# Performance work log

Measured on AMD Instinct MI355X. Metric: run time of the kernel, lower is better.

The kernel has to match this reference:

```python
import jax, jax.numpy as jnp
import numpy as np

B, TQ, TK, D = 16, 1024, 4096, 512


def setup_inputs() -> dict:
    key = jax.random.key(0)
    k1, k2, k3 = jax.random.split(key, 3)
    decoder_output = jax.random.normal(k1, (B, TQ, D), dtype=jnp.float32)
    encoder_output = jax.random.normal(k2, (B, TK, D), dtype=jnp.float32)
    # Keras Dense(lstm_size): kernel [D, D] (glorot-ish scale), bias [D] (zeros init)
    W_a = jax.random.normal(k3, (D, D), dtype=jnp.float32) * (1.0 / np.sqrt(D))
    b_a = jnp.zeros((D,), dtype=jnp.float32)
    return {"decoder_output": decoder_output, "encoder_output": encoder_output,
            "W_a": W_a, "b_a": b_a}


def reference(decoder_output, encoder_output, W_a, b_a):
    # Luong 'general' attention:
    # proj = Dense(encoder_output)            [B, Tk, D]
    proj = jnp.einsum('bkd,de->bke', encoder_output, W_a) + b_a
    # score = dec @ proj^T                    [B, Tq, Tk]
    score = jnp.einsum('bqd,bkd->bqk', decoder_output, proj)
    # softmax over encoder time axis (tf axis=2 == last axis here)
    alignment_vector = jax.nn.softmax(score, axis=-1)
    # context = align @ encoder_output        [B, Tq, D]
    context_vector = jnp.einsum('bqk,bkd->bqd', alignment_vector, encoder_output)
    return (context_vector, alignment_vector)
```

## Files before the change

### kernel.cpp

```cpp
#include <hip/hip_runtime.h>
#include <hip/hip_bf16.h>

#define B_  16
#define TQ_ 1024
#define TK_ 4096
#define D_  512

typedef unsigned short u16;
typedef __attribute__((ext_vector_type(8))) short short8;
typedef __attribute__((ext_vector_type(8))) _Float16 f16x8;
typedef __attribute__((ext_vector_type(4))) float f32x4;

__device__ __forceinline__ u16 bf16_rne(float x) {
  unsigned u = __float_as_uint(x);
  u += 0x7FFFu + ((u >> 16) & 1u);
  return (u16)(u >> 16);
}
__device__ __forceinline__ float bf16_as_f32(u16 h) {
  return __uint_as_float(((unsigned)h) << 16);
}
__device__ __forceinline__ void split_bf16(float x, u16& h, u16& l) {
  u16 hh = bf16_rne(x);
  h = hh;
  l = bf16_rne(x - bf16_as_f32(hh));
}

__device__ __forceinline__ void glld16(const void* g, void* lds) {
  __builtin_amdgcn_global_load_lds(
      (const __attribute__((address_space(1))) unsigned int*)g,
      (__attribute__((address_space(3))) unsigned int*)lds, 16, 0, 0);
}

__device__ __forceinline__ int seg_src4(int l) {
  return (l & 3) ^ ((l >> 2) & 3) ^ ((l >> 4) & 3);
}

__global__ __launch_bounds__(256) void split_planes_kernel(
    const float* __restrict__ X, u16* __restrict__ H, u16* __restrict__ L,
    int n8)
{
  int i = blockIdx.x * 256 + threadIdx.x;
  if (i >= n8) return;
  const float4* src = (const float4*)X + (size_t)i * 2;
  float4 a = src[0], b = src[1];
  __align__(16) u16 h[8], l[8];
  split_bf16(a.x, h[0], l[0]);
  split_bf16(a.y, h[1], l[1]);
  split_bf16(a.z, h[2], l[2]);
  split_bf16(a.w, h[3], l[3]);
  split_bf16(b.x, h[4], l[4]);
  split_bf16(b.y, h[5], l[5]);
  split_bf16(b.z, h[6], l[6]);
  split_bf16(b.w, h[7], l[7]);
  *(uint4*)&H[(size_t)i * 8] = *(const uint4*)h;
  *(uint4*)&L[(size_t)i * 8] = *(const uint4*)l;
}

__global__ __launch_bounds__(256) void transpose_conv_kernel(
    const float* __restrict__ E, _Float16* __restrict__ ET,
    _Float16* __restrict__ EF)
{
  __shared__ float tile[64][65];
  const int b  = blockIdx.z;
  const int k0 = blockIdx.x * 64;
  const int d0 = blockIdx.y * 64;
  const float* Eb = E + (long long)b * TK_ * D_;
  _Float16* ETb = ET + (long long)b * D_ * TK_;

  const int t  = threadIdx.x;
  const int r  = t >> 2;
  const int c4 = (t & 3) * 16;

  __align__(16) _Float16 g[16];
  #pragma unroll
  for (int i = 0; i < 16; i += 4) {
    float4 v = *(const float4*)&Eb[(long long)(k0 + r) * D_ + d0 + c4 + i];
    tile[r][c4 + i + 0] = v.x;
    tile[r][c4 + i + 1] = v.y;
    tile[r][c4 + i + 2] = v.z;
    tile[r][c4 + i + 3] = v.w;
    g[i + 0] = (_Float16)v.x;
    g[i + 1] = (_Float16)v.y;
    g[i + 2] = (_Float16)v.z;
    g[i + 3] = (_Float16)v.w;
  }
  if (EF) {
    _Float16* EFb = EF + (long long)b * TK_ * D_;
    uint4* dstF = (uint4*)&EFb[(long long)(k0 + r) * D_ + d0 + c4];
    dstF[0] = ((const uint4*)g)[0];
    dstF[1] = ((const uint4*)g)[1];
  }
  __syncthreads();

  __align__(16) _Float16 h[16];
  #pragma unroll
  for (int i = 0; i < 16; ++i) h[i] = (_Float16)tile[c4 + i][r];
  uint4* dst = (uint4*)&ETb[(long long)(d0 + r) * TK_ + k0 + c4];
  dst[0] = ((const uint4*)h)[0];
  dst[1] = ((const uint4*)h)[1];
}

#define D2BM 64
#define D2BN 128
#define D2BK 32

__global__ __launch_bounds__(256) void gemm_dec2p_kernel(
    const u16* __restrict__ Ahp, const u16* __restrict__ Alp,
    const u16* __restrict__ Bhp, const u16* __restrict__ Blp,
    _Float16* __restrict__ Ch, _Float16* __restrict__ Cl)
{
  __shared__ u16 sAh[D2BM * D2BK];
  __shared__ u16 sAl[D2BM * D2BK];
  __shared__ u16 sBh[D2BN * D2BK];
  __shared__ u16 sBl[D2BN * D2BK];

  const int m0 = blockIdx.y * D2BM;
  const int n0 = blockIdx.x * D2BN;

  const int t    = threadIdx.x;
  const int lane = t & 63;
  const int wave = t >> 6;
  const int wrm  = (wave >> 1) * 32;
  const int wcn  = (wave & 1) * 64;
  const int ln   = lane & 15;
  const int qd   = lane >> 4;
  const int sw   = qd ^ (ln & 3) ^ (ln >> 2);

  f32x4 acc[2][4];
  #pragma unroll
  for (int i = 0; i < 2; ++i)
    #pragma unroll
    for (int j = 0; j < 4; ++j) { f32x4 z = {0.f,0.f,0.f,0.f}; acc[i][j] = z; }

  const int ab = seg_src4(lane) * 16;
  const char* gAh = (const char*)Ahp + (long long)(m0 + wave * 16 + (lane >> 2)) * D_ * 2 + ab;
  const char* gAl = (const char*)Alp + (long long)(m0 + wave * 16 + (lane >> 2)) * D_ * 2 + ab;
  const int adst = wave * 1024 + lane * 16;
  const char* gBh = (const char*)Bhp + (long long)(n0 + wave * 32 + (lane >> 2)) * D_ * 2 + ab;
  const char* gBl = (const char*)Blp + (long long)(n0 + wave * 32 + (lane >> 2)) * D_ * 2 + ab;
  const long long rstep = (long long)16 * D_ * 2;
  const int bdst = wave * 2048 + lane * 16;

  for (int k0 = 0; k0 < D_; k0 += D2BK) {
    const long long ko = (long long)k0 * 2;
    glld16(gAh + ko, (char*)sAh + adst);
    glld16(gAl + ko, (char*)sAl + adst);
    glld16(gBh + ko, (char*)sBh + bdst);
    glld16(gBh + ko + rstep, (char*)sBh + bdst + 1024);
    glld16(gBl + ko, (char*)sBl + bdst);
    glld16(gBl + ko + rstep, (char*)sBl + bdst + 1024);
    __syncthreads();

    short8 fah[2], fal[2], fbh[4], fbl[4];
    #pragma unroll
    for (int i = 0; i < 2; ++i) {
      const int ra = (wrm + i * 16 + ln) * D2BK + sw * 8;
      fah[i] = *(const short8*)&sAh[ra];
      fal[i] = *(const short8*)&sAl[ra];
    }
    #pragma unroll
    for (int j = 0; j < 4; ++j) {
      const int rb = (wcn + j * 16 + ln) * D2BK + sw * 8;
      fbh[j] = *(const short8*)&sBh[rb];
      fbl[j] = *(const short8*)&sBl[rb];
    }
    #pragma unroll
    for (int i = 0; i < 2; ++i)
      #pragma unroll
      for (int j = 0; j < 4; ++j) {
        acc[i][j] = __builtin_amdgcn_mfma_f32_16x16x32_bf16(fah[i], fbh[j], acc[i][j], 0, 0, 0);
        acc[i][j] = __builtin_amdgcn_mfma_f32_16x16x32_bf16(fah[i], fbl[j], acc[i][j], 0, 0, 0);
        acc[i][j] = __builtin_amdgcn_mfma_f32_16x16x32_bf16(fal[i], fbh[j], acc[i][j], 0, 0, 0);
      }
    __syncthreads();
  }

  #pragma unroll
  for (int i = 0; i < 2; ++i)
    #pragma unroll
    for (int j = 0; j < 4; ++j)
      #pragma unroll
      for (int rg = 0; rg < 4; ++rg) {
        int row = m0 + wrm + i * 16 + qd * 4 + rg;
        int col = n0 + wcn + j * 16 + ln;
        float x = acc[i][j][rg];
        _Float16 h = (_Float16)x;
        _Float16 l = (_Float16)(x - (float)h);
        long long idx = (long long)row * D_ + col;
        Ch[idx] = h;
        Cl[idx] = l;
      }
}

#define DBM 128
#define DBN 128
#define DBK 32
#define DPAD 40

__global__ __launch_bounds__(256) void gemm_dec2_kernel(
    const float* __restrict__ A, const float* __restrict__ Bm,
    _Float16* __restrict__ Ch, _Float16* __restrict__ Cl)
{
  __shared__ u16 Ah[DBM * DPAD];
  __shared__ u16 Al[DBM * DPAD];
  __shared__ u16 Bh[DBN * DPAD];
  __shared__ u16 Bl[DBN * DPAD];

  const float* Ab = A  + (long long)(blockIdx.y * DBM) * D_;
  const float* Bb = Bm + (long long)(blockIdx.x * DBN) * D_;

  const int t    = threadIdx.x;
  const int r    = t >> 1;
  const int hf   = t & 1;
  const int lane = t & 63;
  const int wave = t >> 6;
  const int wr   = (wave >> 1) * 64;
  const int wc   = (wave & 1) * 64;
  const int ln   = lane & 15;
  const int qd   = lane >> 4;

  f32x4 acc[4][4];
  #pragma unroll
  for (int i = 0; i < 4; ++i)
    #pragma unroll
    for (int j = 0; j < 4; ++j) { f32x4 z = {0.f,0.f,0.f,0.f}; acc[i][j] = z; }

  const float* srcA = Ab + (long long)r * D_ + hf * 16;
  const float* srcB = Bb + (long long)r * D_ + hf * 16;
  u16* dAh = &Ah[r * DPAD + hf * 16];
  u16* dAl = &Al[r * DPAD + hf * 16];
  u16* dBh = &Bh[r * DPAD + hf * 16];
  u16* dBl = &Bl[r * DPAD + hf * 16];

  for (int k0 = 0; k0 < D_; k0 += DBK) {
    {
      __align__(16) u16 h[16], l[16];
      #pragma unroll
      for (int i = 0; i < 16; i += 4) {
        float4 v = *(const float4*)(srcA + k0 + i);
        split_bf16(v.x, h[i+0], l[i+0]);
        split_bf16(v.y, h[i+1], l[i+1]);
        split_bf16(v.z, h[i+2], l[i+2]);
        split_bf16(v.w, h[i+3], l[i+3]);
      }
      ((uint4*)dAh)[0] = ((const uint4*)h)[0];
      ((uint4*)dAh)[1] = ((const uint4*)h)[1];
      ((uint4*)dAl)[0] = ((const uint4*)l)[0];
      ((uint4*)dAl)[1] = ((const uint4*)l)[1];
      #pragma unroll
      for (int i = 0; i < 16; i += 4) {
        float4 v = *(const float4*)(srcB + k0 + i);
        split_bf16(v.x, h[i+0], l[i+0]);
        split_bf16(v.y, h[i+1], l[i+1]);
        split_bf16(v.z, h[i+2], l[i+2]);
        split_bf16(v.w, h[i+3], l[i+3]);
      }
      ((uint4*)dBh)[0] = ((const uint4*)h)[0];
      ((uint4*)dBh)[1] = ((const uint4*)h)[1];
      ((uint4*)dBl)[0] = ((const uint4*)l)[0];
      ((uint4*)dBl)[1] = ((const uint4*)l)[1];
    }
    __syncthreads();

    short8 fah[4], fal[4], fbh[4], fbl[4];
    #pragma unroll
    for (int i = 0; i < 4; ++i) {
      int ra = (wr + i * 16 + ln) * DPAD + qd * 8;
      int rb = (wc + i * 16 + ln) * DPAD + qd * 8;
      fah[i] = *(const short8*)&Ah[ra];
      fal[i] = *(const short8*)&Al[ra];
      fbh[i] = *(const short8*)&Bh[rb];
      fbl[i] = *(const short8*)&Bl[rb];
    }
    #pragma unroll
    for (int i = 0; i < 4; ++i)
      #pragma unroll
      for (int j = 0; j < 4; ++j) {
        acc[i][j] = __builtin_amdgcn_mfma_f32_16x16x32_bf16(fah[i], fbh[j], acc[i][j], 0, 0, 0);
        acc[i][j] = __builtin_amdgcn_mfma_f32_16x16x32_bf16(fah[i], fbl[j], acc[i][j], 0, 0, 0);
        acc[i][j] = __builtin_amdgcn_mfma_f32_16x16x32_bf16(fal[i], fbh[j], acc[i][j], 0, 0, 0);
      }
    __syncthreads();
  }

  const int m0 = blockIdx.y * DBM;
  const int n0 = blockIdx.x * DBN;
  #pragma unroll
  for (int i = 0; i < 4; ++i)
    #pragma unroll
    for (int j = 0; j < 4; ++j)
      #pragma unroll
      for (int rg = 0; rg < 4; ++rg) {
        int row = m0 + wr + i * 16 + qd * 4 + rg;
        int col = n0 + wc + j * 16 + ln;
        float x = acc[i][j][rg];
        _Float16 h = (_Float16)x;
        _Float16 l = (_Float16)(x - (float)h);
        long long idx = (long long)row * D_ + col;
        Ch[idx] = h;
        Cl[idx] = l;
      }
}

#define SBM 128
#define SBN 128
#define SBK 32

template<bool F16B>
__global__ __launch_bounds__(256) void gemm_score_kernel(
    const _Float16* __restrict__ A_h, const _Float16* __restrict__ A_l,
    const float* __restrict__ Bf, const _Float16* __restrict__ B16,
    float* __restrict__ C)
{
  __shared__ _Float16 sAh[SBM * SBK];
  __shared__ _Float16 sAl[SBM * SBK];
  __shared__ _Float16 sB [SBN * SBK];

  const int bz = blockIdx.z;
  const int m0 = blockIdx.y * SBM;
  const int n0 = blockIdx.x * SBN;
  const _Float16* Ahb = A_h + (long long)bz * TQ_ * D_ + (long long)m0 * D_;
  const _Float16* Alb = A_l + (long long)bz * TQ_ * D_ + (long long)m0 * D_;

  const int t    = threadIdx.x;
  const int lane = t & 63;
  const int wave = t >> 6;
  const int wr   = (wave >> 1) * 64;
  const int wc   = (wave & 1) * 64;
  const int ln   = lane & 15;
  const int qd   = lane >> 4;
  const int sw   = qd ^ (ln & 3) ^ (ln >> 2);

  f32x4 acc[4][4];
  #pragma unroll
  for (int i = 0; i < 4; ++i)
    #pragma unroll
    for (int j = 0; j < 4; ++j) { f32x4 z = {0.f,0.f,0.f,0.f}; acc[i][j] = z; }

  const int c0   = wave * 2;
  const int arow = c0 * 16 + (lane >> 2);
  const int ab   = seg_src4(lane) * 16;
  const char* gAh = (const char*)Ahb + (long long)arow * D_ * 2 + ab;
  const char* gAl = (const char*)Alb + (long long)arow * D_ * 2 + ab;
  const long long rstep = (long long)16 * D_ * 2;
  char* lAh = (char*)sAh + c0 * 1024 + lane * 16;
  char* lAl = (char*)sAl + c0 * 1024 + lane * 16;
  char* lB  = (char*)sB  + c0 * 1024 + lane * 16;

  const char* gB16 = nullptr;
  if constexpr (F16B) {
    const _Float16* Bb16 = B16 + (long long)bz * TK_ * D_ + (long long)n0 * D_;
    gB16 = (const char*)Bb16 + (long long)arow * D_ * 2 + ab;
  }

  const float* Bb = Bf + (long long)bz * TK_ * D_ + (long long)n0 * D_;
  const int brow = t >> 1;
  const int bhf  = t & 1;
  const float* srcB = Bb + (long long)brow * D_ + bhf * 16;
  const int bh2 = (brow & 3) ^ ((brow >> 2) & 3);
  _Float16* dB0 = &sB[brow * SBK + ((2 * bhf    ) ^ bh2) * 8];
  _Float16* dB1 = &sB[brow * SBK + ((2 * bhf + 1) ^ bh2) * 8];

  for (int k0 = 0; k0 < D_; k0 += SBK) {
    glld16(gAh + (long long)k0 * 2, lAh);
    glld16(gAh + (long long)k0 * 2 + rstep, lAh + 1024);
    glld16(gAl + (long long)k0 * 2, lAl);
    glld16(gAl + (long long)k0 * 2 + rstep, lAl + 1024);
    if constexpr (F16B) {
      glld16(gB16 + (long long)k0 * 2, lB);
      glld16(gB16 + (long long)k0 * 2 + rstep, lB + 1024);
    } else {
      __align__(16) _Float16 hb[16];
      #pragma unroll
      for (int i = 0; i < 16; i += 4) {
        float4 v = *(const float4*)(srcB + k0 + i);
        hb[i+0] = (_Float16)v.x;
        hb[i+1] = (_Float16)v.y;
        hb[i+2] = (_Float16)v.z;
        hb[i+3] = (_Float16)v.w;
      }
      *(uint4*)dB0 = ((const uint4*)hb)[0];
      *(uint4*)dB1 = ((const uint4*)hb)[1];
    }
    __syncthreads();

    f16x8 fah[4], fal[4], fb[4];
    #pragma unroll
    for (int i = 0; i < 4; ++i) {
      int ra = (wr + i * 16 + ln) * SBK + sw * 8;
      int rb = (wc + i * 16 + ln) * SBK + sw * 8;
      fah[i] = *(const f16x8*)&sAh[ra];
      fal[i] = *(const f16x8*)&sAl[ra];
      fb[i]  = *(const f16x8*)&sB[rb];
    }
    #pragma unroll
    for (int i = 0; i < 4; ++i)
      #pragma unroll
      for (int j = 0; j < 4; ++j) {
        acc[i][j] = __builtin_amdgcn_mfma_f32_16x16x32_f16(fah[i], fb[j], acc[i][j], 0, 0, 0);
        acc[i][j] = __builtin_amdgcn_mfma_f32_16x16x32_f16(fal[i], fb[j], acc[i][j], 0, 0, 0);
      }
    __syncthreads();
  }

  float* Cb = C + (long long)bz * TQ_ * TK_;
  #pragma unroll
  for (int i = 0; i < 4; ++i)
    #pragma unroll
    for (int j = 0; j < 4; ++j)
      #pragma unroll
      for (int rg = 0; rg < 4; ++rg) {
        int row = m0 + wr + i * 16 + qd * 4 + rg;
        int col = n0 + wc + j * 16 + ln;
        Cb[(long long)row * TK_ + col] = acc[i][j][rg];
      }
}

template<bool WP16>
__global__ __launch_bounds__(256) void softmax_kernel(
    float* __restrict__ P, _Float16* __restrict__ P16)
{
  __shared__ float red[8];
  float* p = P + (long long)blockIdx.x * TK_;
  const int t    = threadIdx.x;
  const int lane = t & 63;
  const int wave = t >> 6;

  float4 v[4];
  float mx = -3.0e38f;
  #pragma unroll
  for (int i = 0; i < 4; ++i) {
    v[i] = *(const float4*)&p[i * 1024 + t * 4];
    mx = fmaxf(mx, fmaxf(fmaxf(v[i].x, v[i].y), fmaxf(v[i].z, v[i].w)));
  }
  #pragma unroll
  for (int o = 32; o > 0; o >>= 1) mx = fmaxf(mx, __shfl_xor(mx, o, 64));
  if (lane == 0) red[wave] = mx;
  __syncthreads();
  mx = fmaxf(fmaxf(red[0], red[1]), fmaxf(red[2], red[3]));

  float s = 0.f;
  #pragma unroll
  for (int i = 0; i < 4; ++i) {
    v[i].x = __expf(v[i].x - mx);
    v[i].y = __expf(v[i].y - mx);
    v[i].z = __expf(v[i].z - mx);
    v[i].w = __expf(v[i].w - mx);
    s += (v[i].x + v[i].y) + (v[i].z + v[i].w);
  }
  #pragma unroll
  for (int o = 32; o > 0; o >>= 1) s += __shfl_xor(s, o, 64);
  if (lane == 0) red[4 + wave] = s;
  __syncthreads();
  s = (red[4] + red[5]) + (red[6] + red[7]);
  const float inv = 1.0f / s;

  _Float16* p16 = WP16 ? (P16 + (long long)blockIdx.x * TK_) : nullptr;
  #pragma unroll
  for (int i = 0; i < 4; ++i) {
    v[i].x *= inv; v[i].y *= inv; v[i].z *= inv; v[i].w *= inv;
    *(float4*)&p[i * 1024 + t * 4] = v[i];
    if constexpr (WP16) {
      union { _Float16 h[4]; uint2 u; } pk;
      pk.h[0] = (_Float16)v[i].x;
      pk.h[1] = (_Float16)v[i].y;
      pk.h[2] = (_Float16)v[i].z;
      pk.h[3] = (_Float16)v[i].w;
      *(uint2*)&p16[i * 1024 + t * 4] = pk.u;
    }
  }
}

#define CBM 64
#define CBN 128
#define CBK 32
#define C_NT (TK_ / CBK)

template<bool F16A>
__global__ __launch_bounds__(256) void gemm_ctx_kernel(
    const float* __restrict__ P, const _Float16* __restrict__ P16,
    const _Float16* __restrict__ ET, float* __restrict__ C)
{
  __shared__ _Float16 sA[3][CBM * CBK];
  __shared__ _Float16 sB[3][CBN * CBK];

  const int bid = blockIdx.x;
  const int s   = (bid & 7) * 128 + (bid >> 3);
  const int m0  = (s & 15) * CBM;
  const int n0  = ((s >> 4) & 3) * CBN;
  const int bz  = s >> 6;

  const float*    Pb = P  + (long long)bz * TQ_ * TK_ + (long long)m0 * TK_;
  const _Float16* Eb = ET + (long long)bz * D_ * TK_  + (long long)n0 * TK_;

  const int t    = threadIdx.x;
  const int lane = t & 63;
  const int wave = t >> 6;
  const int wr   = (wave >> 1) * 32;
  const int wc   = (wave & 1) * 64;
  const int ln   = lane & 15;
  const int qd   = lane >> 4;
  const int sw   = qd ^ (ln & 3) ^ (ln >> 2);

  f32x4 acc[2][4];
  #pragma unroll
  for (int i = 0; i < 2; ++i)
    #pragma unroll
    for (int j = 0; j < 4; ++j) { f32x4 z = {0.f,0.f,0.f,0.f}; acc[i][j] = z; }

  const int ab = seg_src4(lane) * 16;
  const char* gB = (const char*)Eb + ((long long)(wave * 32 + (lane >> 2)) * TK_) * 2 + ab;
  const long long rstepB = (long long)16 * TK_ * 2;
  const int bdst = wave * 2048 + lane * 16;
  const char* gA16 = nullptr;
  if constexpr (F16A) {
    const _Float16* Pb16 = P16 + (long long)bz * TQ_ * TK_ + (long long)m0 * TK_;
    gA16 = (const char*)Pb16 + ((long long)(wave * 16 + (lane >> 2)) * TK_) * 2 + ab;
  }
  const int adst = wave * 1024 + lane * 16;

  const int arowf = t >> 2;
  const int asegf = t & 3;
  const float* gAf = Pb + (long long)arowf * TK_ + asegf * 8;
  const int afoff = arowf * CBK + ((asegf ^ (arowf & 3) ^ ((arowf >> 2) & 3)) * 8);

  auto stage = [&](int buf, int k0) {
    const long long ko = (long long)k0 * 2;
    char* dB = (char*)sB[buf] + bdst;
    glld16(gB + ko, dB);
    glld16(gB + ko + rstepB, dB + 1024);
    if constexpr (F16A) {
      glld16(gA16 + ko, (char*)sA[buf] + adst);
    } else {
      float4 v0 = *(const float4*)(gAf + k0);
      float4 v1 = *(const float4*)(gAf + k0 + 4);
      __align__(16) _Float16 hb[8];
      hb[0] = (_Float16)v0.x; hb[1] = (_Float16)v0.y;
      hb[2] = (_Float16)v0.z; hb[3] = (_Float16)v0.w;
      hb[4] = (_Float16)v1.x; hb[5] = (_Float16)v1.y;
      hb[6] = (_Float16)v1.z; hb[7] = (_Float16)v1.w;
      *(uint4*)&sA[buf][afoff] = *(const uint4*)hb;
    }
  };

  stage(0, 0);
  stage(1, CBK);
  if constexpr (F16A) {
    asm volatile("s_waitcnt vmcnt(3)" ::: "memory");
  } else {
    asm volatile("s_waitcnt vmcnt(0) lgkmcnt(0)" ::: "memory");
  }
  __builtin_amdgcn_s_barrier();
  __builtin_amdgcn_sched_barrier(0);

  int cur = 0, nxt = 2;
  #pragma unroll 1
  for (int tt = 0; tt < C_NT; ++tt) {
    if (tt + 2 < C_NT) stage(nxt, (tt + 2) * CBK);

    const _Float16* bA  = sA[cur];
    const _Float16* bBv = sB[cur];
    f16x8 fa[2], fb[4];
    #pragma unroll
    for (int i = 0; i < 2; ++i)
      fa[i] = *(const f16x8*)&bA[(wr + i * 16 + ln) * CBK + sw * 8];
    #pragma unroll
    for (int j = 0; j < 4; ++j)
      fb[j] = *(const f16x8*)&bBv[(wc + j * 16 + ln) * CBK + sw * 8];
    __builtin_amdgcn_s_setprio(1);
    #pragma unroll
    for (int i = 0; i < 2; ++i)
      #pragma unroll
      for (int j = 0; j < 4; ++j)
        acc[i][j] = __builtin_amdgcn_mfma_f32_16x16x32_f16(fa[i], fb[j], acc[i][j], 0, 0, 0);
    __builtin_amdgcn_s_setprio(0);
    if (tt + 1 < C_NT) {
      if constexpr (F16A) {
        if (tt + 2 < C_NT) {
          asm volatile("s_waitcnt vmcnt(3)" ::: "memory");
        } else {
          asm volatile("s_waitcnt vmcnt(0)" ::: "memory");
        }
      } else {
        asm volatile("s_waitcnt vmcnt(0) lgkmcnt(0)" ::: "memory");
      }
      __builtin_amdgcn_s_barrier();
      __builtin_amdgcn_sched_barrier(0);
    }
    cur = (cur == 2) ? 0 : cur + 1;
    nxt = (nxt == 2) ? 0 : nxt + 1;
  }

  float* Cb = C + (long long)bz * TQ_ * D_;
  #pragma unroll
  for (int i = 0; i < 2; ++i)
    #pragma unroll
    for (int j = 0; j < 4; ++j)
      #pragma unroll
      for (int rg = 0; rg < 4; ++rg) {
        int row = m0 + wr + i * 16 + qd * 4 + rg;
        int col = n0 + wc + j * 16 + ln;
        Cb[(long long)row * D_ + col] = acc[i][j][rg];
      }
}

extern "C" void kernel_launch(void* const* d_in, const int* in_sizes, int n_in,
                              void* d_out, int out_size, void* d_ws, size_t ws_size,
                              hipStream_t stream) {
  (void)in_sizes; (void)n_in; (void)out_size;
  const float* dec = (const float*)d_in[0];
  const float* enc = (const float*)d_in[1];
  const float* Wa  = (const float*)d_in[2];

  float* ctx   = (float*)d_out;
  float* align = ctx + (long long)B_ * TQ_ * D_;

  char* ws = (char*)d_ws;
  const size_t SZ_ENCT = (size_t)B_ * D_ * TK_ * 2;
  const size_t SZ_DEC2 = (size_t)B_ * TQ_ * D_ * 2;
  const size_t SZ_ENCF = (size_t)B_ * TK_ * D_ * 2;
  const size_t SZ_P16  = (size_t)B_ * TQ_ * TK_ * 2;
  const size_t SZ_WB   = (size_t)D_ * D_ * 2;

  _Float16* encT  = (_Float16*)(ws);
  _Float16* dec2h = (_Float16*)(ws + SZ_ENCT);
  _Float16* dec2l = (_Float16*)(ws + SZ_ENCT + SZ_DEC2);
  _Float16* encF  = (_Float16*)(ws + SZ_ENCT + 2 * SZ_DEC2);
  _Float16* p16   = (_Float16*)(ws + SZ_ENCT);
  u16* dech = (u16*)(ws + SZ_ENCT + SZ_P16);
  u16* decl = dech + (size_t)B_ * TQ_ * D_;
  u16* Wh   = decl + (size_t)B_ * TQ_ * D_;
  u16* Wl   = Wh + (size_t)D_ * D_;

  const bool mid  = ws_size >= SZ_ENCT + 2 * SZ_DEC2 + SZ_ENCF;
  const bool full = ws_size >= SZ_ENCT + SZ_P16;
  const bool pre  = ws_size >= SZ_ENCT + SZ_P16 + 2 * SZ_DEC2 + 2 * SZ_WB;

  transpose_conv_kernel<<<dim3(TK_ / 64, D_ / 64, B_), 256, 0, stream>>>(
      enc, encT, mid ? encF : nullptr);

  if (pre) {
    split_planes_kernel<<<dim3((B_ * TQ_ * D_ / 8) / 256), 256, 0, stream>>>(
        dec, dech, decl, B_ * TQ_ * D_ / 8);
    split_planes_kernel<<<dim3((D_ * D_ / 8) / 256), 256, 0, stream>>>(
        Wa, Wh, Wl, D_ * D_ / 8);
    gemm_dec2p_kernel<<<dim3(D_ / D2BN, (B_ * TQ_) / D2BM), 256, 0, stream>>>(
        dech, decl, Wh, Wl, dec2h, dec2l);
  } else {
    gemm_dec2_kernel<<<dim3(D_ / DBN, (B_ * TQ_) / DBM), 256, 0, stream>>>(
        dec, Wa, dec2h, dec2l);
  }

  if (mid)
    gemm_score_kernel<true><<<dim3(TK_ / SBN, TQ_ / SBM, B_), 256, 0, stream>>>(
        dec2h, dec2l, enc, encF, align);
  else
    gemm_score_kernel<false><<<dim3(TK_ / SBN, TQ_ / SBM, B_), 256, 0, stream>>>(
        dec2h, dec2l, enc, nullptr, align);

  if (full)
    softmax_kernel<true><<<B_ * TQ_, 256, 0, stream>>>(align, p16);
  else
    softmax_kernel<false><<<B_ * TQ_, 256, 0, stream>>>(align, nullptr);

  if (full)
    gemm_ctx_kernel<true><<<dim3((TQ_ / CBM) * (D_ / CBN) * B_), 256, 0, stream>>>(
        align, p16, encT, ctx);
  else
    gemm_ctx_kernel<false><<<dim3((TQ_ / CBM) * (D_ / CBN) * B_), 256, 0, stream>>>(
        align, nullptr, encT, ctx);
}
```

Before: 853.0 us.

## Double-buffer LDS tiles in decoder-projection and score GEMMs

```diff
diff --git a/kernel.cpp b/kernel.cpp
--- a/kernel.cpp
+++ b/kernel.cpp
@@ -103,16 +103,17 @@
 #define D2BM 64
 #define D2BN 128
 #define D2BK 32
+#define D2NT (D_ / D2BK)
 
 __global__ __launch_bounds__(256) void gemm_dec2p_kernel(
     const u16* __restrict__ Ahp, const u16* __restrict__ Alp,
     const u16* __restrict__ Bhp, const u16* __restrict__ Blp,
     _Float16* __restrict__ Ch, _Float16* __restrict__ Cl)
 {
-  __shared__ u16 sAh[D2BM * D2BK];
-  __shared__ u16 sAl[D2BM * D2BK];
-  __shared__ u16 sBh[D2BN * D2BK];
-  __shared__ u16 sBl[D2BN * D2BK];
+  __shared__ u16 sAh[2][D2BM * D2BK];
+  __shared__ u16 sAl[2][D2BM * D2BK];
+  __shared__ u16 sBh[2][D2BN * D2BK];
+  __shared__ u16 sBl[2][D2BN * D2BK];
 
   const int m0 = blockIdx.y * D2BM;
   const int n0 = blockIdx.x * D2BN;
@@ -141,29 +142,39 @@
   const long long rstep = (long long)16 * D_ * 2;
   const int bdst = wave * 2048 + lane * 16;
 
-  for (int k0 = 0; k0 < D_; k0 += D2BK) {
+  auto stage = [&](int buf, int k0) {
     const long long ko = (long long)k0 * 2;
-    glld16(gAh + ko, (char*)sAh + adst);
-    glld16(gAl + ko, (char*)sAl + adst);
-    glld16(gBh + ko, (char*)sBh + bdst);
-    glld16(gBh + ko + rstep, (char*)sBh + bdst + 1024);
-    glld16(gBl + ko, (char*)sBl + bdst);
-    glld16(gBl + ko + rstep, (char*)sBl + bdst + 1024);
-    __syncthreads();
+    glld16(gAh + ko, (char*)sAh[buf] + adst);
+    glld16(gAl + ko, (char*)sAl[buf] + adst);
+    glld16(gBh + ko, (char*)sBh[buf] + bdst);
+    glld16(gBh + ko + rstep, (char*)sBh[buf] + bdst + 1024);
+    glld16(gBl + ko, (char*)sBl[buf] + bdst);
+    glld16(gBl + ko + rstep, (char*)sBl[buf] + bdst + 1024);
+  };
+
+  stage(0, 0);
+  __syncthreads();
+
+  #pragma unroll
+  for (int tt = 0; tt < D2NT; ++tt) {
+    const int cur = tt & 1;
+    if (tt + 1 < D2NT) stage(cur ^ 1, (tt + 1) * D2BK);
+    __builtin_amdgcn_sched_barrier(0);
 
     short8 fah[2], fal[2], fbh[4], fbl[4];
     #pragma unroll
     for (int i = 0; i < 2; ++i) {
       const int ra = (wrm + i * 16 + ln) * D2BK + sw * 8;
-      fah[i] = *(const short8*)&sAh[ra];
-      fal[i] = *(const short8*)&sAl[ra];
+      fah[i] = *(const short8*)&sAh[cur][ra];
+      fal[i] = *(const short8*)&sAl[cur][ra];
     }
     #pragma unroll
     for (int j = 0; j < 4; ++j) {
       const int rb = (wcn + j * 16 + ln) * D2BK + sw * 8;
-      fbh[j] = *(const short8*)&sBh[rb];
-      fbl[j] = *(const short8*)&sBl[rb];
-    }
+      fbh[j] = *(const short8*)&sBh[cur][rb];
+      fbl[j] = *(const short8*)&sBl[cur][rb];
+    }
+    __builtin_amdgcn_s_setprio(1);
     #pragma unroll
     for (int i = 0; i < 2; ++i)
       #pragma unroll
@@ -172,6 +183,7 @@
         acc[i][j] = __builtin_amdgcn_mfma_f32_16x16x32_bf16(fah[i], fbl[j], acc[i][j], 0, 0, 0);
         acc[i][j] = __builtin_amdgcn_mfma_f32_16x16x32_bf16(fal[i], fbh[j], acc[i][j], 0, 0, 0);
       }
+    __builtin_amdgcn_s_setprio(0);
     __syncthreads();
   }
 
@@ -305,6 +317,7 @@
 #define SBM 128
 #define SBN 128
 #define SBK 32
+#define S_NT (D_ / SBK)
 
 template<bool F16B>
 __global__ __launch_bounds__(256) void gemm_score_kernel(
@@ -312,9 +325,9 @@
     const float* __restrict__ Bf, const _Float16* __restrict__ B16,
     float* __restrict__ C)
 {
-  __shared__ _Float16 sAh[SBM * SBK];
-  __shared__ _Float16 sAl[SBM * SBK];
-  __shared__ _Float16 sB [SBN * SBK];
+  __shared__ _Float16 sAh[2][SBM * SBK];
+  __shared__ _Float16 sAl[2][SBM * SBK];
+  __shared__ _Float16 sB [2][SBN * SBK];
 
   const int bz = blockIdx.z;
   const int m0 = blockIdx.y * SBM;
@@ -343,9 +356,7 @@
   const char* gAh = (const char*)Ahb + (long long)arow * D_ * 2 + ab;
   const char* gAl = (const char*)Alb + (long long)arow * D_ * 2 + ab;
   const long long rstep = (long long)16 * D_ * 2;
-  char* lAh = (char*)sAh + c0 * 1024 + lane * 16;
-  char* lAl = (char*)sAl + c0 * 1024 + lane * 16;
-  char* lB  = (char*)sB  + c0 * 1024 + lane * 16;
+  const int dstoff = c0 * 1024 + lane * 16;
 
   const char* gB16 = nullptr;
   if constexpr (F16B) {
@@ -358,17 +369,21 @@
   const int bhf  = t & 1;
   const float* srcB = Bb + (long long)brow * D_ + bhf * 16;
   const int bh2 = (brow & 3) ^ ((brow >> 2) & 3);
-  _Float16* dB0 = &sB[brow * SBK + ((2 * bhf    ) ^ bh2) * 8];
-  _Float16* dB1 = &sB[brow * SBK + ((2 * bhf + 1) ^ bh2) * 8];
-
-  for (int k0 = 0; k0 < D_; k0 += SBK) {
-    glld16(gAh + (long long)k0 * 2, lAh);
-    glld16(gAh + (long long)k0 * 2 + rstep, lAh + 1024);
-    glld16(gAl + (long long)k0 * 2, lAl);
-    glld16(gAl + (long long)k0 * 2 + rstep, lAl + 1024);
+  const int db0 = brow * SBK + ((2 * bhf    ) ^ bh2) * 8;
+  const int db1 = brow * SBK + ((2 * bhf + 1) ^ bh2) * 8;
+
+  auto stage = [&](int buf, int k0) {
+    const long long ko = (long long)k0 * 2;
+    char* dAh = (char*)sAh[buf] + dstoff;
+    char* dAl = (char*)sAl[buf] + dstoff;
+    glld16(gAh + ko, dAh);
+    glld16(gAh + ko + rstep, dAh + 1024);
+    glld16(gAl + ko, dAl);
+    glld16(gAl + ko + rstep, dAl + 1024);
     if constexpr (F16B) {
-      glld16(gB16 + (long long)k0 * 2, lB);
-      glld16(gB16 + (long long)k0 * 2 + rstep, lB + 1024);
+      char* dBv = (char*)sB[buf] + dstoff;
+      glld16(gB16 + ko, dBv);
+      glld16(gB16 + ko + rstep, dBv + 1024);
     } else {
       __align__(16) _Float16 hb[16];
       #pragma unroll
@@ -379,20 +394,30 @@
         hb[i+2] = (_Float16)v.z;
         hb[i+3] = (_Float16)v.w;
       }
-      *(uint4*)dB0 = ((const uint4*)hb)[0];
-      *(uint4*)dB1 = ((const uint4*)hb)[1];
-    }
-    __syncthreads();
+      *(uint4*)&sB[buf][db0] = ((const uint4*)hb)[0];
+      *(uint4*)&sB[buf][db1] = ((const uint4*)hb)[1];
+    }
+  };
+
+  stage(0, 0);
+  __syncthreads();
+
+  #pragma unroll
+  for (int tt = 0; tt < S_NT; ++tt) {
+    const int cur = tt & 1;
+    if (tt + 1 < S_NT) stage(cur ^ 1, (tt + 1) * SBK);
+    __builtin_amdgcn_sched_barrier(0);
 
     f16x8 fah[4], fal[4], fb[4];
     #pragma unroll
     for (int i = 0; i < 4; ++i) {
-      int ra = (wr + i * 16 + ln) * SBK + sw * 8;
-      int rb = (wc + i * 16 + ln) * SBK + sw * 8;
-      fah[i] = *(const f16x8*)&sAh[ra];
-      fal[i] = *(const f16x8*)&sAl[ra];
-      fb[i]  = *(const f16x8*)&sB[rb];
-    }
+      const int ra = (wr + i * 16 + ln) * SBK + sw * 8;
+      const int rb = (wc + i * 16 + ln) * SBK + sw * 8;
+      fah[i] = *(const f16x8*)&sAh[cur][ra];
+      fal[i] = *(const f16x8*)&sAl[cur][ra];
+      fb[i]  = *(const f16x8*)&sB[cur][rb];
+    }
+    __builtin_amdgcn_s_setprio(1);
     #pragma unroll
     for (int i = 0; i < 4; ++i)
       #pragma unroll
@@ -400,6 +425,7 @@
         acc[i][j] = __builtin_amdgcn_mfma_f32_16x16x32_f16(fah[i], fb[j], acc[i][j], 0, 0, 0);
         acc[i][j] = __builtin_amdgcn_mfma_f32_16x16x32_f16(fal[i], fb[j], acc[i][j], 0, 0, 0);
       }
+    __builtin_amdgcn_s_setprio(0);
     __syncthreads();
   }
 
```

Measured after the change: 850.8 us. No clear change (-0.3%).
